# Kernel tuning notes

Hardware: AMD Instinct MI355X
Metric: run time of the kernel (lower is better)

The kernel has to match this reference:

```python
import jax, jax.numpy as jnp
import numpy as np

B, S, E, H, D, W = 2, 4096, 512, 8, 64, 512
NUM_BUCKETS, MAX_DISTANCE = 32, 128  # hardcoded in get_relative_positions for 't5'
NEG_INF = -1e30


def _t5_bucket_causal(relative_position):
    """T5 relative position bucketing, unidirectional (causal)."""
    n = jnp.maximum(-relative_position, 0)
    max_exact = NUM_BUCKETS // 2
    is_small = n < max_exact
    nf = jnp.maximum(n.astype(jnp.float32), 1.0)
    val_if_large = max_exact + (
        jnp.log(nf / max_exact) / np.log(MAX_DISTANCE / max_exact)
        * (NUM_BUCKETS - max_exact)
    ).astype(jnp.int32)
    val_if_large = jnp.minimum(val_if_large, NUM_BUCKETS - 1)
    return jnp.where(is_small, n, val_if_large)


def setup_inputs() -> dict:
    key = jax.random.key(0)
    ks = jax.random.split(key, 7)
    scale = 1.0 / np.sqrt(E)  # keep logits in a sane range
    return {
        'xs': jax.random.normal(ks[0], (B, S, E), jnp.float32),
        'prev_k': jax.random.normal(ks[1], (B, W, H, D), jnp.float32),
        'prev_v': jax.random.normal(ks[2], (B, W, H, D), jnp.float32),
        'w_q': jax.random.normal(ks[3], (E, H, D), jnp.float32) * scale,
        'w_k': jax.random.normal(ks[4], (E, H, D), jnp.float32) * scale,
        'w_v': jax.random.normal(ks[5], (E, H, D), jnp.float32) * scale,
        'rel_bias': jax.random.normal(ks[6], (H, NUM_BUCKETS), jnp.float32),
    }


def reference(xs, prev_k, prev_v, w_q, w_k, w_v, rel_bias):
    nw = S // W  # number of windows
    # kvq projections; queries pre-scaled by 1/sqrt(head_size)
    q = jnp.einsum('bse,ehd->bshd', xs, w_q) * (1.0 / np.sqrt(D))
    k = jnp.einsum('bse,ehd->bshd', xs, w_k)
    v = jnp.einsum('bse,ehd->bshd', xs, w_v)
    qw = q.reshape(B, nw, W, H, D)
    kw = k.reshape(B, nw, W, H, D)
    vw = v.reshape(B, nw, W, H, D)
    # Transformer-XL sliding window: keys for window i = [window i-1 keys ; window i keys]
    k_prev = jnp.concatenate([prev_k[:, None], kw[:, :-1]], axis=1)  # (B,nw,W,H,D)
    v_prev = jnp.concatenate([prev_v[:, None], vw[:, :-1]], axis=1)
    k2 = jnp.concatenate([k_prev, kw], axis=2)  # (B,nw,2W,H,D)
    v2 = jnp.concatenate([v_prev, vw], axis=2)
    # T5 relative position bias and causal mask (num_queries=W, num_keys=2W)
    ctx = jnp.arange(W)[:, None] + W          # query absolute position in key frame
    mem = jnp.arange(2 * W)[None, :]
    relpos = mem - ctx                        # (W, 2W), key - query
    bias = rel_bias[:, _t5_bucket_causal(relpos)]  # (H, W, 2W)
    # causal + window mask: key j attends iff i < j <= i+W (each query sees exactly W keys)
    mask = (relpos <= 0) & (relpos > -W)
    # attention per window
    scores = jnp.einsum('bnqhd,bnkhd->bnhqk', qw, k2)  # (B,nw,H,W,2W)
    scores = scores + bias[None, None]
    scores = jnp.where(mask[None, None, None], scores, NEG_INF)
    probs = jax.nn.softmax(scores, axis=-1)
    attn = jnp.einsum('bnhqk,bnkhd->bnqhd', probs, v2)
    attn_ys = attn.reshape(B, S, H, D)
    # next_kvi cache = last window's keys/values
    next_k = kw[:, -1]
    next_v = vw[:, -1]
    return attn_ys, next_k, next_v
```

## Files before the change

### kernel.cpp

```cpp
#include <hip/hip_runtime.h>
#include <hip/hip_bf16.h>
#include <math.h>

#define B_ 2
#define S_ 4096
#define H_ 8
#define D_ 64
#define W_ 512

#define MASKV -1e30f
#define LOG2E 1.4426950408889634f

typedef float f32x4 __attribute__((ext_vector_type(4)));
typedef short s16x4 __attribute__((ext_vector_type(4)));
typedef short s16x8 __attribute__((ext_vector_type(8)));
typedef unsigned int u32;
typedef unsigned int u32x2 __attribute__((ext_vector_type(2)));
typedef __attribute__((address_space(1))) const u32 as1_u32;
typedef __attribute__((address_space(3))) u32 as3_u32;

__device__ inline short f2bf(float f) {
    unsigned u = __builtin_bit_cast(unsigned, f);
    unsigned r = (u + 0x7FFFu + ((u >> 16) & 1u)) >> 16;
    return (short)r;
}
__device__ inline s16x8 pack8(f32x4 a, f32x4 b) {
    s16x8 r;
    r[0]=f2bf(a[0]); r[1]=f2bf(a[1]); r[2]=f2bf(a[2]); r[3]=f2bf(a[3]);
    r[4]=f2bf(b[0]); r[5]=f2bf(b[1]); r[6]=f2bf(b[2]); r[7]=f2bf(b[3]);
    return r;
}
__device__ __forceinline__ u32 cvtpk_bf16(float a, float b) {
    u32 r;
    asm("v_cvt_pk_bf16_f32 %0, %1, %2" : "=v"(r) : "v"(a), "v"(b));
    return r;
}
__device__ __forceinline__ float fexp2(float x) {
    float r;
    asm("v_exp_f32 %0, %1" : "=v"(r) : "v"(x));
    return r;
}
__device__ __forceinline__ void gl_lds16(const void* g, void* l) {
    __builtin_amdgcn_global_load_lds((as1_u32*)(unsigned long long)g,
                                     (as3_u32*)(u32)(unsigned long long)l,
                                     16, 0, 0);
}
__device__ __forceinline__ void drain_vmem() {
    asm volatile("s_waitcnt vmcnt(0)" ::: "memory");
}

__global__ __launch_bounds__(256, 4)
void prep_kernel(const float* __restrict__ xs, const float* __restrict__ pk,
                 const float* __restrict__ pv, const float* __restrict__ wq,
                 const float* __restrict__ wk, const float* __restrict__ wv,
                 short* __restrict__ xsbf, short* __restrict__ pkbf,
                 short* __restrict__ vbt, short* __restrict__ wt)
{
    __shared__ char smem[17408];
    const int bid = blockIdx.x;
    const int tid = threadIdx.x;

    if (bid < 2304) {
        size_t i8 = ((size_t)bid * 256 + tid) * 8;
        const float* src; short* dst; size_t off;
        if (i8 < 4194304) { src = xs; dst = xsbf; off = i8; }
        else              { src = pk; dst = pkbf; off = i8 - 4194304; }
        f32x4 a = *(const f32x4*)(src + off);
        f32x4 b = *(const f32x4*)(src + off + 4);
        *(s16x8*)(dst + off) = pack8(a, b);
    } else if (bid < 2432) {
        short (*st)[72] = (short(*)[72])smem;
        const int b2 = bid - 2304;
        const int jt = b2 & 7, h = (b2 >> 3) & 7, b = b2 >> 6;
        const int jj0 = jt * 64;
        {
            int kk = tid >> 2, d0 = (tid & 3) * 16;
            const float* src = pv + (((size_t)(b * 512 + jj0 + kk)) * 8 + h) * 64 + d0;
            f32x4 x0 = *(const f32x4*)(src);
            f32x4 x1 = *(const f32x4*)(src + 4);
            f32x4 x2 = *(const f32x4*)(src + 8);
            f32x4 x3 = *(const f32x4*)(src + 12);
            *(s16x8*)&st[kk][d0]     = pack8(x0, x1);
            *(s16x8*)&st[kk][d0 + 8] = pack8(x2, x3);
        }
        __syncthreads();
        {
            int dd = tid >> 2, k0 = (tid & 3) * 16;
            s16x8 o0, o1;
            #pragma unroll
            for (int t = 0; t < 8; ++t) { o0[t] = st[k0 + t][dd]; o1[t] = st[k0 + 8 + t][dd]; }
            short* dst = vbt + (size_t)(h * 64 + dd) * 9216 + b * 4608 + jj0 + k0;
            *(s16x8*)dst = o0;
            *(s16x8*)(dst + 8) = o1;
        }
    } else {
        float (*st)[68] = (float(*)[68])smem;
        const int t2 = bid - 2432;
        const int k0 = (t2 & 7) * 64;
        const int nt = t2 >> 3;
        const int z  = nt >> 3;
        const int n0 = (nt & 7) * 64;
        const float* wz = (z == 0) ? wq : (z == 1) ? wk : wv;
        const float scale = (z == 0) ? 0.125f * LOG2E : 1.0f;
        {
            int kk = tid >> 4, nn = (tid & 15) * 4;
            #pragma unroll
            for (int it = 0; it < 4; ++it) {
                f32x4 x = *(const f32x4*)(wz + (size_t)(k0 + kk + it * 16) * 512 + n0 + nn);
                *(f32x4*)&st[kk + it * 16][nn] = x;
            }
        }
        __syncthreads();
        {
            int nn2 = tid >> 2, kseg = (tid & 3) * 16;
            s16x8 o0, o1;
            #pragma unroll
            for (int j = 0; j < 8; ++j) o0[j] = f2bf(st[kseg + j][nn2] * scale);
            #pragma unroll
            for (int j = 0; j < 8; ++j) o1[j] = f2bf(st[kseg + 8 + j][nn2] * scale);
            short* dst = wt + (size_t)(z * 512 + n0 + nn2) * 512 + k0 + kseg;
            *(s16x8*)(dst) = o0;
            *(s16x8*)(dst + 8) = o1;
        }
    }
}

__global__ __launch_bounds__(256, 4)
void proj_kernel(const short* __restrict__ xsbf, const short* __restrict__ wt,
                 short* __restrict__ qkbf, short* __restrict__ vbt,
                 float* __restrict__ out)
{
    __shared__ short Xs[2][128][32];
    __shared__ short Ws[2][128][32];

    const int tid = threadIdx.x;
    const int m0  = blockIdx.x * 128;
    const int n0  = blockIdx.y * 128;
    const int z   = n0 >> 9;
    const int ln0 = n0 & 511;
    const int wave = tid >> 6, lane = tid & 63;
    const int wq = (wave & 1) * 64;
    const int wx = (wave >> 1) * 64;
    const int lr = lane & 15, quad = lane >> 4;

    f32x4 acc[4][4] = {};

    const int r4 = lane >> 2;
    const int g4 = lane & 3;

    auto stage = [&](int s, int buf) {
        const int k0 = s * 32;
        #pragma unroll
        for (int i = 0; i < 2; ++i) {
            int row = 32 * wave + 16 * i + r4;
            int gs  = g4 ^ (row & 3);
            gl_lds16(xsbf + (size_t)(m0 + row) * 512 + k0 + gs * 8,
                     &Xs[buf][32 * wave + 16 * i][0]);
            gl_lds16(wt   + (size_t)(n0 + row) * 512 + k0 + gs * 8,
                     &Ws[buf][32 * wave + 16 * i][0]);
        }
    };

    stage(0, 0);
    for (int s = 0; s < 16; ++s) {
        const int buf = s & 1;
        drain_vmem();
        __syncthreads();
        if (s < 15) stage(s + 1, buf ^ 1);

        s16x8 af[4], bf[4];
        #pragma unroll
        for (int ta = 0; ta < 4; ++ta) {
            int R = wq + ta * 16 + lr;
            af[ta] = *(const s16x8*)&Ws[buf][R][((quad ^ (R & 3)) * 8)];
        }
        #pragma unroll
        for (int tb = 0; tb < 4; ++tb) {
            int R = wx + tb * 16 + lr;
            bf[tb] = *(const s16x8*)&Xs[buf][R][((quad ^ (R & 3)) * 8)];
        }
        #pragma unroll
        for (int ta = 0; ta < 4; ++ta)
            #pragma unroll
            for (int tb = 0; tb < 4; ++tb)
                acc[ta][tb] = __builtin_amdgcn_mfma_f32_16x16x32_bf16(
                    af[ta], bf[tb], acc[ta][tb], 0, 0, 0);
    }

    #pragma unroll
    for (int ta = 0; ta < 4; ++ta)
        #pragma unroll
        for (int tb = 0; tb < 4; ++tb) {
            int m  = m0 + wx + tb * 16 + lr;
            int ln = ln0 + wq + ta * 16 + quad * 4;
            int bb = m >> 12, seq = m & 4095;
            if (z < 2) {
                short* base = qkbf + (size_t)z * ((size_t)8192 * 512);
                u32x2 o;
                o[0] = cvtpk_bf16(acc[ta][tb][0], acc[ta][tb][1]);
                o[1] = cvtpk_bf16(acc[ta][tb][2], acc[ta][tb][3]);
                *(u32x2*)(base + (size_t)m * 512 + ln) = o;
                if (z == 1 && seq >= 3584) {
                    float* dst = out + 4194304 + ((size_t)(bb * 512 + seq - 3584)) * 512 + ln;
                    *(f32x4*)dst = acc[ta][tb];
                }
            } else {
                size_t col = (size_t)bb * 4608 + 512 + seq;
                #pragma unroll
                for (int g = 0; g < 4; ++g)
                    vbt[(size_t)(ln + g) * 9216 + col] = f2bf(acc[ta][tb][g]);
                if (seq >= 3584) {
                    float* dst = out + 4194304 + 524288 + ((size_t)(bb * 512 + seq - 3584)) * 512 + ln;
                    *(f32x4*)dst = acc[ta][tb];
                }
            }
        }
}

__global__ __launch_bounds__(512, 4)
void attn_kernel(const short* __restrict__ qkbf, const short* __restrict__ vbt,
                 const short* __restrict__ pkbf, const float* __restrict__ rel_bias,
                 float* __restrict__ out)
{
    __shared__ short k_s[2][64][64];
    __shared__ short vt_s[2][64][64];
    __shared__ short p_s[128][64];
    __shared__ float bias_s[512];

    const short* qb = qkbf;
    const short* kb = qkbf + (size_t)8192 * 512;

    const int bid = blockIdx.x;
    const int qt = bid & 3;
    const int h  = (bid >> 2) & 7;
    const int n  = (bid >> 5) & 7;
    const int b  = bid >> 8;
    const int tid = threadIdx.x;
    const int wave = tid >> 6, lane = tid & 63;
    const int lr = lane & 15, quad = lane >> 4;
    const int q0 = qt * 128;
    const int i0 = q0 + 16 * wave;

    {
        int nd = tid;
        int bucket;
        if (nd < 16) bucket = nd;
        else {
            int vbk = 16 + (int)(log((double)nd * (1.0 / 16.0)) * (16.0 / log(8.0)));
            bucket = vbk < 31 ? vbk : 31;
        }
        bias_s[nd] = rel_bias[h * 32 + bucket] * LOG2E;
    }
    const float bias31 = rel_bias[h * 32 + 31] * LOG2E;

    s16x8 aq[2];
    {
        const short* src = qb + (size_t)(b * S_ + n * W_ + i0 + lr) * 512 + h * 64 + quad * 8;
        aq[0] = *(const s16x8*)(src);
        aq[1] = *(const s16x8*)(src + 32);
    }

    f32x4 oacc[4] = {};
    float lsum = 0.f;

    const int cmin = (16 * wave) >> 6;
    const int cmax = (16 * wave + 527) >> 6;

    const int r8 = lane >> 3, gr = lane & 7;

    auto issueKV = [&](int c, int pb) {
        int jj = q0 + 64 * c + 8 * wave + r8;
        int p  = n * W_ + jj - W_;
        int gs = gr ^ r8;
        const short* ksrc = (p >= 0)
            ? kb   + ((size_t)(b * S_ + p)) * 512 + h * 64 + gs * 8
            : pkbf + (((size_t)(b * W_ + jj)) * 8 + h) * 64 + gs * 8;
        gl_lds16(ksrc, &k_s[pb][8 * wave][0]);
        int drow = 8 * wave + r8;
        const short* vsrc = vbt + (size_t)(h * 64 + drow) * 9216
                          + b * 4608 + n * W_ + q0 + 64 * c + gs * 8;
        gl_lds16(vsrc, &vt_s[pb][8 * wave][0]);
    };

    issueKV(0, 0);

    for (int c = 0; c < 10; ++c) {
        const int pb = c & 1;
        drain_vmem();
        __syncthreads();
        if (c < 9) issueKV(c + 1, pb ^ 1);
        if (c < cmin || c > cmax) continue;

        f32x4 sacc[4] = {};
        #pragma unroll
        for (int ks = 0; ks < 2; ++ks) {
            s16x8 bk[4];
            #pragma unroll
            for (int tn = 0; tn < 4; ++tn)
                bk[tn] = *(const s16x8*)&k_s[pb][tn * 16 + lr][(((4 * ks + quad) ^ (lr & 7)) * 8)];
            #pragma unroll
            for (int tn = 0; tn < 4; ++tn)
                sacc[tn] = __builtin_amdgcn_mfma_f32_16x16x32_bf16(
                    bk[tn], aq[ks], sacc[tn], 0, 0, 0);
        }

        const int ib = i0 + lr;
        const int jb = q0 + 64 * c;
        if (64 * c - 16 * wave <= 336) {
            #pragma unroll
            for (int tn = 0; tn < 4; ++tn) {
                float pv[4];
                #pragma unroll
                for (int rg = 0; rg < 4; ++rg) {
                    int j = jb + tn * 16 + quad * 4 + rg;
                    unsigned dm1 = (unsigned)(j - ib - 1);
                    float sv = (dm1 < 512u) ? (sacc[tn][rg] + bias31) : MASKV;
                    float p = fexp2(sv);
                    lsum += p;
                    pv[rg] = p;
                }
                u32x2 pp;
                pp[0] = cvtpk_bf16(pv[0], pv[1]);
                pp[1] = cvtpk_bf16(pv[2], pv[3]);
                int gp = (2 * tn + (quad >> 1)) ^ (lr & 7);
                *(u32x2*)&p_s[16 * wave + lr][gp * 8 + (quad & 1) * 4] = pp;
            }
        } else {
            #pragma unroll
            for (int tn = 0; tn < 4; ++tn) {
                float pv[4];
                #pragma unroll
                for (int rg = 0; rg < 4; ++rg) {
                    int j = jb + tn * 16 + quad * 4 + rg;
                    unsigned dm1 = (unsigned)(j - ib - 1);
                    float bias = bias_s[(ib + 512 - j) & 511];
                    float sv = (dm1 < 512u) ? (sacc[tn][rg] + bias) : MASKV;
                    float p = fexp2(sv);
                    lsum += p;
                    pv[rg] = p;
                }
                u32x2 pp;
                pp[0] = cvtpk_bf16(pv[0], pv[1]);
                pp[1] = cvtpk_bf16(pv[2], pv[3]);
                int gp = (2 * tn + (quad >> 1)) ^ (lr & 7);
                *(u32x2*)&p_s[16 * wave + lr][gp * 8 + (quad & 1) * 4] = pp;
            }
        }

        asm volatile("s_waitcnt lgkmcnt(0)" ::: "memory");

        #pragma unroll
        for (int ks = 0; ks < 2; ++ks) {
            int gpa = (4 * ks + quad) ^ (lr & 7);
            s16x8 ap = *(const s16x8*)&p_s[16 * wave + lr][gpa * 8];
            s16x8 bv[4];
            #pragma unroll
            for (int tn = 0; tn < 4; ++tn)
                bv[tn] = *(const s16x8*)&vt_s[pb][tn * 16 + lr][(((4 * ks + quad) ^ (lr & 7)) * 8)];
            #pragma unroll
            for (int tn = 0; tn < 4; ++tn)
                oacc[tn] = __builtin_amdgcn_mfma_f32_16x16x32_bf16(
                    ap, bv[tn], oacc[tn], 0, 0, 0);
        }
    }

    lsum += __shfl_xor(lsum, 16);
    lsum += __shfl_xor(lsum, 32);
    float linv[4];
    #pragma unroll
    for (int rg = 0; rg < 4; ++rg)
        linv[rg] = 1.0f / __shfl(lsum, quad * 4 + rg);

    #pragma unroll
    for (int rg = 0; rg < 4; ++rg) {
        int row = i0 + quad * 4 + rg;
        float* dst = out + (((size_t)b * S_ + n * W_ + row) * H_ + h) * D_ + lr;
        #pragma unroll
        for (int tn = 0; tn < 4; ++tn)
            dst[tn * 16] = oacc[tn][rg] * linv[rg];
    }
}

extern "C" void kernel_launch(void* const* d_in, const int* in_sizes, int n_in,
                              void* d_out, int out_size, void* d_ws, size_t ws_size,
                              hipStream_t stream)
{
    const float* xs       = (const float*)d_in[0];
    const float* prev_k   = (const float*)d_in[1];
    const float* prev_v   = (const float*)d_in[2];
    const float* w_q      = (const float*)d_in[3];
    const float* w_k      = (const float*)d_in[4];
    const float* w_v      = (const float*)d_in[5];
    const float* rel_bias = (const float*)d_in[6];
    float* out = (float*)d_out;

    short* xsbf = (short*)d_ws;
    short* wt   = xsbf + (size_t)4194304;
    short* qkbf = wt   + (size_t)786432;
    short* pkbf = qkbf + (size_t)8388608;
    short* vbt  = pkbf + (size_t)524288;

    prep_kernel<<<2624, 256, 0, stream>>>(xs, prev_k, prev_v, w_q, w_k, w_v,
                                          xsbf, pkbf, vbt, wt);

    proj_kernel<<<dim3(64, 12), 256, 0, stream>>>(xsbf, wt, qkbf, vbt, out);

    attn_kernel<<<512, 512, 0, stream>>>(qkbf, vbt, pkbf, rel_bias, out);
}
```

Before: 131.3 us.

## Fuse xs bf16 conversion into projection, triple-buffer attention KV loads, remap blocks

The separate fp32->bf16 pass over xs in the prep kernel is removed. The projection kernel now loads fp32 xs through registers, converts it and writes the bf16 tile to LDS itself, which avoids a workspace round trip and shrinks the prep grid. The attention kernel goes from double to triple buffering of K/V tiles with a partial vmcnt wait, keeping two loads in flight. Block indices are also remapped so that blocks sharing a group are spread across XCDs. In exchange, projection launch bounds drop to 3 waves per SIMD, X loads become register-staged rather than direct-to-LDS, and LDS use in attention grows.

After: 133.5 us. Within noise of the previous version (+1.7%).

```diff
diff --git a/kernel.cpp b/kernel.cpp
--- a/kernel.cpp
+++ b/kernel.cpp
@@ -16,6 +16,7 @@
 typedef short s16x8 __attribute__((ext_vector_type(8)));
 typedef unsigned int u32;
 typedef unsigned int u32x2 __attribute__((ext_vector_type(2)));
+typedef unsigned int u32x4 __attribute__((ext_vector_type(4)));
 typedef __attribute__((address_space(1))) const u32 as1_u32;
 typedef __attribute__((address_space(3))) u32 as3_u32;
 
@@ -45,32 +46,26 @@
                                      (as3_u32*)(u32)(unsigned long long)l,
                                      16, 0, 0);
 }
-__device__ __forceinline__ void drain_vmem() {
-    asm volatile("s_waitcnt vmcnt(0)" ::: "memory");
-}
 
 __global__ __launch_bounds__(256, 4)
-void prep_kernel(const float* __restrict__ xs, const float* __restrict__ pk,
-                 const float* __restrict__ pv, const float* __restrict__ wq,
-                 const float* __restrict__ wk, const float* __restrict__ wv,
-                 short* __restrict__ xsbf, short* __restrict__ pkbf,
-                 short* __restrict__ vbt, short* __restrict__ wt)
+void prep_kernel(const float* __restrict__ pk, const float* __restrict__ pv,
+                 const float* __restrict__ wq, const float* __restrict__ wk,
+                 const float* __restrict__ wv,
+                 short* __restrict__ pkbf, short* __restrict__ vbt,
+                 short* __restrict__ wt)
 {
     __shared__ char smem[17408];
     const int bid = blockIdx.x;
     const int tid = threadIdx.x;
 
-    if (bid < 2304) {
+    if (bid < 256) {
         size_t i8 = ((size_t)bid * 256 + tid) * 8;
-        const float* src; short* dst; size_t off;
-        if (i8 < 4194304) { src = xs; dst = xsbf; off = i8; }
-        else              { src = pk; dst = pkbf; off = i8 - 4194304; }
-        f32x4 a = *(const f32x4*)(src + off);
-        f32x4 b = *(const f32x4*)(src + off + 4);
-        *(s16x8*)(dst + off) = pack8(a, b);
-    } else if (bid < 2432) {
+        f32x4 a = *(const f32x4*)(pk + i8);
+        f32x4 b = *(const f32x4*)(pk + i8 + 4);
+        *(s16x8*)(pkbf + i8) = pack8(a, b);
+    } else if (bid < 384) {
         short (*st)[72] = (short(*)[72])smem;
-        const int b2 = bid - 2304;
+        const int b2 = bid - 256;
         const int jt = b2 & 7, h = (b2 >> 3) & 7, b = b2 >> 6;
         const int jj0 = jt * 64;
         {
@@ -95,7 +90,7 @@
         }
     } else {
         float (*st)[68] = (float(*)[68])smem;
-        const int t2 = bid - 2432;
+        const int t2 = bid - 384;
         const int k0 = (t2 & 7) * 64;
         const int nt = t2 >> 3;
         const int z  = nt >> 3;
@@ -125,8 +120,8 @@
     }
 }
 
-__global__ __launch_bounds__(256, 4)
-void proj_kernel(const short* __restrict__ xsbf, const short* __restrict__ wt,
+__global__ __launch_bounds__(256, 3)
+void proj_kernel(const float* __restrict__ xs, const short* __restrict__ wt,
                  short* __restrict__ qkbf, short* __restrict__ vbt,
                  float* __restrict__ out)
 {
@@ -148,25 +143,49 @@
     const int r4 = lane >> 2;
     const int g4 = lane & 3;
 
-    auto stage = [&](int s, int buf) {
+    auto stageW = [&](int s, int buf) {
         const int k0 = s * 32;
         #pragma unroll
         for (int i = 0; i < 2; ++i) {
             int row = 32 * wave + 16 * i + r4;
             int gs  = g4 ^ (row & 3);
-            gl_lds16(xsbf + (size_t)(m0 + row) * 512 + k0 + gs * 8,
-                     &Xs[buf][32 * wave + 16 * i][0]);
-            gl_lds16(wt   + (size_t)(n0 + row) * 512 + k0 + gs * 8,
+            gl_lds16(wt + (size_t)(n0 + row) * 512 + k0 + gs * 8,
                      &Ws[buf][32 * wave + 16 * i][0]);
         }
     };
-
-    stage(0, 0);
+    f32x4 xr[4];
+    auto loadX = [&](int s) {
+        const int k0 = s * 32;
+        #pragma unroll
+        for (int i = 0; i < 2; ++i) {
+            int row = 32 * wave + 16 * i + r4;
+            int gs  = g4 ^ (row & 3);
+            const float* p = xs + (size_t)(m0 + row) * 512 + k0 + gs * 8;
+            xr[2 * i]     = *(const f32x4*)(p);
+            xr[2 * i + 1] = *(const f32x4*)(p + 4);
+        }
+    };
+    auto writeX = [&](int buf) {
+        #pragma unroll
+        for (int i = 0; i < 2; ++i) {
+            int row = 32 * wave + 16 * i + r4;
+            u32x4 o;
+            o[0] = cvtpk_bf16(xr[2*i][0],   xr[2*i][1]);
+            o[1] = cvtpk_bf16(xr[2*i][2],   xr[2*i][3]);
+            o[2] = cvtpk_bf16(xr[2*i+1][0], xr[2*i+1][1]);
+            o[3] = cvtpk_bf16(xr[2*i+1][2], xr[2*i+1][3]);
+            *(u32x4*)&Xs[buf][row][g4 * 8] = o;
+        }
+    };
+
+    stageW(0, 0);
+    loadX(0);
+    writeX(0);
+    __syncthreads();
+
     for (int s = 0; s < 16; ++s) {
         const int buf = s & 1;
-        drain_vmem();
-        __syncthreads();
-        if (s < 15) stage(s + 1, buf ^ 1);
+        if (s < 15) { stageW(s + 1, buf ^ 1); loadX(s + 1); }
 
         s16x8 af[4], bf[4];
         #pragma unroll
@@ -185,6 +204,11 @@
             for (int tb = 0; tb < 4; ++tb)
                 acc[ta][tb] = __builtin_amdgcn_mfma_f32_16x16x32_bf16(
                     af[ta], bf[tb], acc[ta][tb], 0, 0, 0);
+
+        if (s < 15) {
+            writeX(buf ^ 1);
+            __syncthreads();
+        }
     }
 
     #pragma unroll
@@ -222,8 +246,8 @@
                  const short* __restrict__ pkbf, const float* __restrict__ rel_bias,
                  float* __restrict__ out)
 {
-    __shared__ short k_s[2][64][64];
-    __shared__ short vt_s[2][64][64];
+    __shared__ short k_s[3][64][64];
+    __shared__ short vt_s[3][64][64];
     __shared__ short p_s[128][64];
     __shared__ float bias_s[512];
 
@@ -231,10 +255,13 @@
     const short* kb = qkbf + (size_t)8192 * 512;
 
     const int bid = blockIdx.x;
-    const int qt = bid & 3;
-    const int h  = (bid >> 2) & 7;
-    const int n  = (bid >> 5) & 7;
-    const int b  = bid >> 8;
+    const int slot = bid >> 3;
+    const int qt  = slot & 3;
+    const int grp = (bid & 7) * 16 + (slot >> 2);
+    const int h = grp & 7;
+    const int n = (grp >> 3) & 7;
+    const int b = grp >> 6;
+
     const int tid = threadIdx.x;
     const int wave = tid >> 6, lane = tid & 63;
     const int lr = lane & 15, quad = lane >> 4;
@@ -282,13 +309,17 @@
         gl_lds16(vsrc, &vt_s[pb][8 * wave][0]);
     };
 
+    __syncthreads();
     issueKV(0, 0);
+    issueKV(1, 1);
 
     for (int c = 0; c < 10; ++c) {
-        const int pb = c & 1;
-        drain_vmem();
-        __syncthreads();
-        if (c < 9) issueKV(c + 1, pb ^ 1);
+        const int pb = c % 3;
+        if (c < 9) { asm volatile("s_waitcnt vmcnt(2)" ::: "memory"); }
+        else       { asm volatile("s_waitcnt vmcnt(0)" ::: "memory"); }
+        __builtin_amdgcn_s_barrier();
+        __builtin_amdgcn_sched_barrier(0);
+        if (c < 8) issueKV(c + 2, (c + 2) % 3);
         if (c < cmin || c > cmax) continue;
 
         f32x4 sacc[4] = {};
@@ -394,16 +425,15 @@
     const float* rel_bias = (const float*)d_in[6];
     float* out = (float*)d_out;
 
-    short* xsbf = (short*)d_ws;
-    short* wt   = xsbf + (size_t)4194304;
+    short* wt   = (short*)d_ws;
     short* qkbf = wt   + (size_t)786432;
     short* pkbf = qkbf + (size_t)8388608;
     short* vbt  = pkbf + (size_t)524288;
 
-    prep_kernel<<<2624, 256, 0, stream>>>(xs, prev_k, prev_v, w_q, w_k, w_v,
-                                          xsbf, pkbf, vbt, wt);
-
-    proj_kernel<<<dim3(64, 12), 256, 0, stream>>>(xsbf, wt, qkbf, vbt, out);
+    prep_kernel<<<576, 256, 0, stream>>>(prev_k, prev_v, w_q, w_k, w_v,
+                                         pkbf, vbt, wt);
+
+    proj_kernel<<<dim3(64, 12), 256, 0, stream>>>(xs, wt, qkbf, vbt, out);
 
     attn_kernel<<<512, 512, 0, stream>>>(qkbf, vbt, pkbf, rel_bias, out);
 }
```

## Replace double-buffered K32 projection staging with single-buffer K64 tiles

Applied to the files above, without the earlier changes.

The projection GEMM drops its two-stage double-buffered LDS pipeline with 32-wide K slices. It now uses a single buffer of 64-wide K slices, loaded and then consumed with two MFMA sub-steps per barrier. This halves the number of iterations and barriers and uses an 8-way XOR swizzle for the wider rows. In exchange, global loads no longer overlap with MFMA compute, and each iteration adds a second barrier.

Result: faster. 127.5 us (-2.9%).

```diff
diff --git a/kernel.cpp b/kernel.cpp
--- a/kernel.cpp
+++ b/kernel.cpp
@@ -130,8 +130,8 @@
                  short* __restrict__ qkbf, short* __restrict__ vbt,
                  float* __restrict__ out)
 {
-    __shared__ short Xs[2][128][32];
-    __shared__ short Ws[2][128][32];
+    __shared__ short Xs[128][64];
+    __shared__ short Ws[128][64];
 
     const int tid = threadIdx.x;
     const int m0  = blockIdx.x * 128;
@@ -145,46 +145,40 @@
 
     f32x4 acc[4][4] = {};
 
-    const int r4 = lane >> 2;
-    const int g4 = lane & 3;
-
-    auto stage = [&](int s, int buf) {
-        const int k0 = s * 32;
-        #pragma unroll
-        for (int i = 0; i < 2; ++i) {
-            int row = 32 * wave + 16 * i + r4;
-            int gs  = g4 ^ (row & 3);
-            gl_lds16(xsbf + (size_t)(m0 + row) * 512 + k0 + gs * 8,
-                     &Xs[buf][32 * wave + 16 * i][0]);
-            gl_lds16(wt   + (size_t)(n0 + row) * 512 + k0 + gs * 8,
-                     &Ws[buf][32 * wave + 16 * i][0]);
-        }
-    };
-
-    stage(0, 0);
-    for (int s = 0; s < 16; ++s) {
-        const int buf = s & 1;
+    const int r8  = lane >> 3;
+    const int gr  = lane & 7;
+
+    for (int k0 = 0; k0 < 512; k0 += 64) {
+        #pragma unroll
+        for (int i = 0; i < 4; ++i) {
+            int row = 32 * wave + 8 * i + r8;
+            int gs  = gr ^ (row & 7);
+            gl_lds16(xsbf + (size_t)(m0 + row) * 512 + k0 + gs * 8, &Xs[32 * wave + 8 * i][0]);
+            gl_lds16(wt   + (size_t)(n0 + row) * 512 + k0 + gs * 8, &Ws[32 * wave + 8 * i][0]);
+        }
         drain_vmem();
         __syncthreads();
-        if (s < 15) stage(s + 1, buf ^ 1);
-
-        s16x8 af[4], bf[4];
-        #pragma unroll
-        for (int ta = 0; ta < 4; ++ta) {
-            int R = wq + ta * 16 + lr;
-            af[ta] = *(const s16x8*)&Ws[buf][R][((quad ^ (R & 3)) * 8)];
-        }
-        #pragma unroll
-        for (int tb = 0; tb < 4; ++tb) {
-            int R = wx + tb * 16 + lr;
-            bf[tb] = *(const s16x8*)&Xs[buf][R][((quad ^ (R & 3)) * 8)];
-        }
-        #pragma unroll
-        for (int ta = 0; ta < 4; ++ta)
-            #pragma unroll
-            for (int tb = 0; tb < 4; ++tb)
-                acc[ta][tb] = __builtin_amdgcn_mfma_f32_16x16x32_bf16(
-                    af[ta], bf[tb], acc[ta][tb], 0, 0, 0);
+        #pragma unroll
+        for (int ks = 0; ks < 2; ++ks) {
+            s16x8 af[4], bf[4];
+            #pragma unroll
+            for (int ta = 0; ta < 4; ++ta) {
+                int R = wq + ta * 16 + lr;
+                af[ta] = *(const s16x8*)&Ws[R][(((ks * 4 + quad) ^ (R & 7)) * 8)];
+            }
+            #pragma unroll
+            for (int tb = 0; tb < 4; ++tb) {
+                int R = wx + tb * 16 + lr;
+                bf[tb] = *(const s16x8*)&Xs[R][(((ks * 4 + quad) ^ (R & 7)) * 8)];
+            }
+            #pragma unroll
+            for (int ta = 0; ta < 4; ++ta)
+                #pragma unroll
+                for (int tb = 0; tb < 4; ++tb)
+                    acc[ta][tb] = __builtin_amdgcn_mfma_f32_16x16x32_bf16(
+                        af[ta], bf[tb], acc[ta][tb], 0, 0, 0);
+        }
+        __syncthreads();
     }
 
     #pragma unroll
```
